# Kernel tuning notes

Measured on AMD Instinct MI355X. Metric: run time of the kernel, lower is better.

## Reference

```python
import jax, jax.numpy as jnp
import numpy as np


def setup_inputs() -> dict:
    key = jax.random.key(0)
    k1, k2, k3, k4, k5, k6 = jax.random.split(key, 6)
    N, D, K = 8192, 1024, 64
    return {
        "x1": jax.random.normal(k1, (N, D), dtype=jnp.float32),
        "x2": jax.random.normal(k2, (1, D), dtype=jnp.float32),
        "V": jax.random.normal(k3, (K, 2 * D), dtype=jnp.float32) * 0.02,
        "W": jax.random.normal(k4, (K, D, D), dtype=jnp.float32) * 0.02,
        "b": jax.random.normal(k5, (K,), dtype=jnp.float32),
        "U": jax.random.normal(k6, (K, 1), dtype=jnp.float32) * 0.1,
    }


def reference(x1, x2, V, W, b, U):
    # x1: (N, D), x2: (1, D)
    # V term: per slice i, [x1 | tile(x2)] @ V[i] -> fused as one GEMM (N, K)
    cat = jnp.concatenate([x1, jnp.broadcast_to(x2, x1.shape)], axis=1)  # (N, 2D)
    v_term = cat @ V.T  # (N, K)
    # W bilinear term: x1 @ W[i] @ x2^T for each i. Contract x2 into W first
    # (K*D*D flops) then one (N,D)x(D,K) GEMM -- same math, efficient order.
    Wx2 = jnp.einsum('kde,e->kd', W, x2[0])  # (K, D)
    w_term = x1 @ Wx2.T  # (N, K)
    feat = jax.nn.relu(v_term + w_term + b)  # (N, K)
    return feat @ U  # (N, 1)
```

## Files before the change

kernel.cpp:

```cpp
#include <hip/hip_runtime.h>

#define D 1024
#define K 64
#define NROWS 8192

__global__ __launch_bounds__(256) void k1_wx2(
    const float* __restrict__ W, const float* __restrict__ V,
    const float* __restrict__ x2, const float* __restrict__ b,
    float* __restrict__ M, float* __restrict__ c) {
  __shared__ float xsh[D];
  int t = threadIdx.x;
  ((float4*)xsh)[t] = ((const float4*)x2)[t];
  __syncthreads();

  int lane = t & 63;
  int wv = t >> 6;
  long row = (long)blockIdx.x * 4 + wv;
  const long WROWS = (long)K * D;

  const float* src;
  bool is_w = (row < WROWS);
  if (is_w) {
    src = W + row * D;
  } else {
    long k = row - WROWS;
    if (k >= K) return;
    src = V + k * (2 * D) + D;
  }

  const float4* s4 = (const float4*)src;
  const float4* x4 = (const float4*)xsh;
  float sum = 0.f;
#pragma unroll
  for (int it = 0; it < 4; ++it) {
    float4 w = s4[lane + it * 64];
    float4 xv = x4[lane + it * 64];
    sum += w.x * xv.x + w.y * xv.y + w.z * xv.z + w.w * xv.w;
  }
#pragma unroll
  for (int off = 32; off; off >>= 1) sum += __shfl_down(sum, off, 64);

  if (lane == 0) {
    if (is_w) {
      long k = row >> 10;
      long d = row & (D - 1);
      M[row] = sum + V[k * (2 * D) + d];
    } else {
      long k = row - WROWS;
      c[k] = sum + b[k];
    }
  }
}

template <int SPLIT>
__global__ __launch_bounds__(256) void k2_gemm(
    const float* __restrict__ x1, const float* __restrict__ M,
    const float* __restrict__ c, const float* __restrict__ U,
    float* __restrict__ dst) {
  __shared__ float xs[32][68];
  __shared__ float ms[32][68];
  int t = threadIdx.x;

  int nt, d0, dn;
  if (SPLIT) {
    nt = blockIdx.x >> 1;
    d0 = (blockIdx.x & 1) * (D / 2);
    dn = D / 2;
  } else {
    nt = blockIdx.x;
    d0 = 0;
    dn = D;
  }
  int n_base = nt * 64;
  int tx = t & 15, ty = t >> 4;
  int ld_n = t >> 2, ld_f = t & 3;

  const float4* x1v = (const float4*)(x1 + (long)(n_base + ld_n) * D + d0);
  const float4* Mv = (const float4*)(M + (long)ld_n * D + d0);

  float acc[4][4];
#pragma unroll
  for (int i = 0; i < 4; ++i)
#pragma unroll
    for (int j = 0; j < 4; ++j) acc[i][j] = 0.f;

  for (int dc = 0; dc < dn; dc += 32) {
    int cb = dc >> 2;
#pragma unroll
    for (int h = 0; h < 2; ++h) {
      int f4 = ld_f + h * 4;
      float4 xv = x1v[cb + f4];
      float4 mv = Mv[cb + f4];
      int dd = f4 * 4;
      xs[dd + 0][ld_n] = xv.x; xs[dd + 1][ld_n] = xv.y;
      xs[dd + 2][ld_n] = xv.z; xs[dd + 3][ld_n] = xv.w;
      ms[dd + 0][ld_n] = mv.x; ms[dd + 1][ld_n] = mv.y;
      ms[dd + 2][ld_n] = mv.z; ms[dd + 3][ld_n] = mv.w;
    }
    __syncthreads();
#pragma unroll
    for (int d = 0; d < 32; ++d) {
      float4 xv = *(const float4*)&xs[d][ty << 2];
      float4 mv = *(const float4*)&ms[d][tx << 2];
      float xa[4] = {xv.x, xv.y, xv.z, xv.w};
      float ma[4] = {mv.x, mv.y, mv.z, mv.w};
#pragma unroll
      for (int i = 0; i < 4; ++i)
#pragma unroll
        for (int j = 0; j < 4; ++j) acc[i][j] = fmaf(xa[i], ma[j], acc[i][j]);
    }
    __syncthreads();
  }

  if (SPLIT) {
    float* p = dst + (long)(blockIdx.x & 1) * NROWS * K;
#pragma unroll
    for (int i = 0; i < 4; ++i) {
      float4 v = {acc[i][0], acc[i][1], acc[i][2], acc[i][3]};
      *(float4*)&p[(long)(n_base + (ty << 2) + i) * K + (tx << 2)] = v;
    }
  } else {
    float cv[4], uv[4];
#pragma unroll
    for (int j = 0; j < 4; ++j) {
      cv[j] = c[(tx << 2) + j];
      uv[j] = U[(tx << 2) + j];
    }
#pragma unroll
    for (int i = 0; i < 4; ++i) {
      float r = 0.f;
#pragma unroll
      for (int j = 0; j < 4; ++j)
        r += fmaxf(acc[i][j] + cv[j], 0.f) * uv[j];
#pragma unroll
      for (int m = 1; m < 16; m <<= 1) r += __shfl_xor(r, m, 64);
      if (tx == 0) dst[n_base + (ty << 2) + i] = r;
    }
  }
}

__global__ __launch_bounds__(256) void k3_reduce(
    const float* __restrict__ partial, const float* __restrict__ c,
    const float* __restrict__ U, float* __restrict__ out) {
  int t = threadIdx.x;
  int lane = t & 63;
  int n = blockIdx.x * 4 + (t >> 6);
  float a = partial[(long)n * K + lane];
  float bh = partial[(long)NROWS * K + (long)n * K + lane];
  float v = fmaxf(a + bh + c[lane], 0.f) * U[lane];
#pragma unroll
  for (int off = 32; off; off >>= 1) v += __shfl_down(v, off, 64);
  if (lane == 0) out[n] = v;
}

extern "C" void kernel_launch(void* const* d_in, const int* in_sizes, int n_in,
                              void* d_out, int out_size, void* d_ws, size_t ws_size,
                              hipStream_t stream) {
  const float* x1 = (const float*)d_in[0];
  const float* x2 = (const float*)d_in[1];
  const float* V = (const float*)d_in[2];
  const float* W = (const float*)d_in[3];
  const float* b = (const float*)d_in[4];
  const float* U = (const float*)d_in[5];
  float* out = (float*)d_out;

  float* M = (float*)d_ws;
  float* c = M + (long)K * D;
  float* partial = c + 64;

  k1_wx2<<<dim3(16400), dim3(256), 0, stream>>>(W, V, x2, b, M, c);

  size_t need_split = (size_t)(K * D + 64 + 2 * NROWS * K) * sizeof(float);
  if (ws_size >= need_split) {
    k2_gemm<1><<<dim3(256), dim3(256), 0, stream>>>(x1, M, c, U, partial);
    k3_reduce<<<dim3(NROWS / 4), dim3(256), 0, stream>>>(partial, c, U, out);
  } else {
    k2_gemm<0><<<dim3(128), dim3(256), 0, stream>>>(x1, M, c, U, out);
  }
}
```

Measured before the change: 404.9 us.

## Enlarge GEMM register tile to 8x8 and split reduction dimension eight ways

The second-stage GEMM now computes a 256x64 output tile per block, with each thread holding an 8x8 accumulator instead of 4x4. The D dimension is split into eight chunks across blocks, so the grid stays at 256 blocks while arithmetic intensity per shared-memory load rises. The reduce kernel sums eight partial slabs before applying bias, ReLU and the U projection. In exchange, partial-result traffic and workspace size grow, and register pressure rises.

```diff
diff --git a/kernel.cpp b/kernel.cpp
--- a/kernel.cpp
+++ b/kernel.cpp
@@ -52,102 +52,90 @@
   }
 }
 
-template <int SPLIT>
-__global__ __launch_bounds__(256) void k2_gemm(
+template <int NSPLIT>
+__global__ __launch_bounds__(256, 3) void k2_gemm(
     const float* __restrict__ x1, const float* __restrict__ M,
-    const float* __restrict__ c, const float* __restrict__ U,
-    float* __restrict__ dst) {
-  __shared__ float xs[32][68];
-  __shared__ float ms[32][68];
+    float* __restrict__ p) {
+  __shared__ float xs[16][256];
+  __shared__ float ms[16][64];
   int t = threadIdx.x;
+  int nt = blockIdx.x / NSPLIT;
+  int sp = blockIdx.x % NSPLIT;
+  const int DSP = D / NSPLIT;
+  int n0 = nt * 256;
+  int d0 = sp * DSP;
 
-  int nt, d0, dn;
-  if (SPLIT) {
-    nt = blockIdx.x >> 1;
-    d0 = (blockIdx.x & 1) * (D / 2);
-    dn = D / 2;
-  } else {
-    nt = blockIdx.x;
-    d0 = 0;
-    dn = D;
-  }
-  int n_base = nt * 64;
-  int tx = t & 15, ty = t >> 4;
-  int ld_n = t >> 2, ld_f = t & 3;
+  int tx = t & 7;
+  int ty = t >> 3;
+  int mk = t & 63;
+  int mg = t >> 6;
 
-  const float4* x1v = (const float4*)(x1 + (long)(n_base + ld_n) * D + d0);
-  const float4* Mv = (const float4*)(M + (long)ld_n * D + d0);
+  const float4* xrow = (const float4*)(x1 + (long)(n0 + t) * D + d0);
+  const float4* mrow = (const float4*)(M + (long)mk * D + d0) + mg;
 
-  float acc[4][4];
+  float acc[8][8];
 #pragma unroll
-  for (int i = 0; i < 4; ++i)
+  for (int i = 0; i < 8; ++i)
 #pragma unroll
-    for (int j = 0; j < 4; ++j) acc[i][j] = 0.f;
+    for (int j = 0; j < 8; ++j) acc[i][j] = 0.f;
 
-  for (int dc = 0; dc < dn; dc += 32) {
-    int cb = dc >> 2;
+#pragma unroll 1
+  for (int dc = 0; dc < DSP; dc += 16) {
 #pragma unroll
-    for (int h = 0; h < 2; ++h) {
-      int f4 = ld_f + h * 4;
-      float4 xv = x1v[cb + f4];
-      float4 mv = Mv[cb + f4];
-      int dd = f4 * 4;
-      xs[dd + 0][ld_n] = xv.x; xs[dd + 1][ld_n] = xv.y;
-      xs[dd + 2][ld_n] = xv.z; xs[dd + 3][ld_n] = xv.w;
-      ms[dd + 0][ld_n] = mv.x; ms[dd + 1][ld_n] = mv.y;
-      ms[dd + 2][ld_n] = mv.z; ms[dd + 3][ld_n] = mv.w;
+    for (int h = 0; h < 4; ++h) {
+      float4 v = xrow[(dc >> 2) + h];
+      xs[h * 4 + 0][t] = v.x;
+      xs[h * 4 + 1][t] = v.y;
+      xs[h * 4 + 2][t] = v.z;
+      xs[h * 4 + 3][t] = v.w;
+    }
+    {
+      float4 v = mrow[dc >> 2];
+      ms[mg * 4 + 0][mk] = v.x;
+      ms[mg * 4 + 1][mk] = v.y;
+      ms[mg * 4 + 2][mk] = v.z;
+      ms[mg * 4 + 3][mk] = v.w;
     }
     __syncthreads();
 #pragma unroll
-    for (int d = 0; d < 32; ++d) {
-      float4 xv = *(const float4*)&xs[d][ty << 2];
-      float4 mv = *(const float4*)&ms[d][tx << 2];
-      float xa[4] = {xv.x, xv.y, xv.z, xv.w};
-      float ma[4] = {mv.x, mv.y, mv.z, mv.w};
+    for (int d = 0; d < 16; ++d) {
+      float4 a0 = *(const float4*)&xs[d][ty * 8];
+      float4 a1 = *(const float4*)&xs[d][ty * 8 + 4];
+      float4 b0 = *(const float4*)&ms[d][tx * 8];
+      float4 b1 = *(const float4*)&ms[d][tx * 8 + 4];
+      float xa[8] = {a0.x, a0.y, a0.z, a0.w, a1.x, a1.y, a1.z, a1.w};
+      float mb[8] = {b0.x, b0.y, b0.z, b0.w, b1.x, b1.y, b1.z, b1.w};
 #pragma unroll
-      for (int i = 0; i < 4; ++i)
+      for (int i = 0; i < 8; ++i)
 #pragma unroll
-        for (int j = 0; j < 4; ++j) acc[i][j] = fmaf(xa[i], ma[j], acc[i][j]);
+        for (int j = 0; j < 8; ++j)
+          acc[i][j] = fmaf(xa[i], mb[j], acc[i][j]);
     }
     __syncthreads();
   }
 
-  if (SPLIT) {
-    float* p = dst + (long)(blockIdx.x & 1) * NROWS * K;
+  float* dst = p + ((long)sp * NROWS + n0 + (long)ty * 8) * K + tx * 8;
 #pragma unroll
-    for (int i = 0; i < 4; ++i) {
-      float4 v = {acc[i][0], acc[i][1], acc[i][2], acc[i][3]};
-      *(float4*)&p[(long)(n_base + (ty << 2) + i) * K + (tx << 2)] = v;
-    }
-  } else {
-    float cv[4], uv[4];
-#pragma unroll
-    for (int j = 0; j < 4; ++j) {
-      cv[j] = c[(tx << 2) + j];
-      uv[j] = U[(tx << 2) + j];
-    }
-#pragma unroll
-    for (int i = 0; i < 4; ++i) {
-      float r = 0.f;
-#pragma unroll
-      for (int j = 0; j < 4; ++j)
-        r += fmaxf(acc[i][j] + cv[j], 0.f) * uv[j];
-#pragma unroll
-      for (int m = 1; m < 16; m <<= 1) r += __shfl_xor(r, m, 64);
-      if (tx == 0) dst[n_base + (ty << 2) + i] = r;
-    }
+  for (int i = 0; i < 8; ++i) {
+    float4 v0 = {acc[i][0], acc[i][1], acc[i][2], acc[i][3]};
+    float4 v1 = {acc[i][4], acc[i][5], acc[i][6], acc[i][7]};
+    *(float4*)&dst[(long)i * K] = v0;
+    *(float4*)&dst[(long)i * K + 4] = v1;
   }
 }
 
+template <int NSPLIT>
 __global__ __launch_bounds__(256) void k3_reduce(
-    const float* __restrict__ partial, const float* __restrict__ c,
+    const float* __restrict__ p, const float* __restrict__ c,
     const float* __restrict__ U, float* __restrict__ out) {
   int t = threadIdx.x;
   int lane = t & 63;
   int n = blockIdx.x * 4 + (t >> 6);
-  float a = partial[(long)n * K + lane];
-  float bh = partial[(long)NROWS * K + (long)n * K + lane];
-  float v = fmaxf(a + bh + c[lane], 0.f) * U[lane];
+  float s = 0.f;
+#pragma unroll
+  for (int sp = 0; sp < NSPLIT; ++sp)
+    s += p[((long)sp * NROWS + n) * K + lane];
+  float v = fmaxf(s + c[lane], 0.f) * U[lane];
 #pragma unroll
   for (int off = 32; off; off >>= 1) v += __shfl_down(v, off, 64);
   if (lane == 0) out[n] = v;
@@ -170,11 +158,12 @@
 
   k1_wx2<<<dim3(16400), dim3(256), 0, stream>>>(W, V, x2, b, M, c);
 
-  size_t need_split = (size_t)(K * D + 64 + 2 * NROWS * K) * sizeof(float);
-  if (ws_size >= need_split) {
-    k2_gemm<1><<<dim3(256), dim3(256), 0, stream>>>(x1, M, c, U, partial);
-    k3_reduce<<<dim3(NROWS / 4), dim3(256), 0, stream>>>(partial, c, U, out);
+  size_t need8 = (size_t)(K * D + 64 + 8L * NROWS * K) * sizeof(float);
+  if (ws_size >= need8) {
+    k2_gemm<8><<<dim3(256), dim3(256), 0, stream>>>(x1, M, partial);
+    k3_reduce<8><<<dim3(NROWS / 4), dim3(256), 0, stream>>>(partial, c, U, out);
   } else {
-    k2_gemm<0><<<dim3(128), dim3(256), 0, stream>>>(x1, M, c, U, out);
+    k2_gemm<1><<<dim3(32), dim3(256), 0, stream>>>(x1, M, partial);
+    k3_reduce<1><<<dim3(NROWS / 4), dim3(256), 0, stream>>>(partial, c, U, out);
   }
 }
```

Result: no change. 404.4 us (-0.1%).
